# Performance work log

Hardware: AMD Instinct MI355X
Metric: run time of the kernel (lower is better)

Reference implementation:

```python
import jax, jax.numpy as jnp
import numpy as np

BN_EPS = 1e-5


def setup_inputs() -> dict:
    key = jax.random.key(0)
    ks = jax.random.split(key, 8)
    B, C, H, W = 8, 256, 64, 64
    Cqk = C // 8  # query/key channels = out_channels // 8
    x = jax.random.normal(ks[0], (B, C, H, W), dtype=jnp.float32)
    # 1x1 convs == per-pixel matmuls; kaiming-normal-ish scale
    wq = jax.random.normal(ks[1], (Cqk, C), dtype=jnp.float32) * np.sqrt(2.0 / C)
    bq = jnp.zeros((Cqk,), dtype=jnp.float32)
    wk = jax.random.normal(ks[2], (Cqk, C), dtype=jnp.float32) * np.sqrt(2.0 / C)
    bk = jnp.zeros((Cqk,), dtype=jnp.float32)
    wv = jax.random.normal(ks[3], (C, C), dtype=jnp.float32) * np.sqrt(2.0 / C)
    bv = jnp.zeros((C,), dtype=jnp.float32)
    # gamma is initialized to 0 in the original; use a small nonzero value so
    # the attention path actually contributes (and has nontrivial gradients)
    gamma = jnp.full((1,), 0.5, dtype=jnp.float32)
    bn_weight = jnp.ones((C,), dtype=jnp.float32)
    bn_bias = jnp.zeros((C,), dtype=jnp.float32)
    return {"x": x, "wq": wq, "bq": bq, "wk": wk, "bk": bk,
            "wv": wv, "bv": bv, "gamma": gamma,
            "bn_weight": bn_weight, "bn_bias": bn_bias}


def reference(x, wq, bq, wk, bk, wv, bv, gamma, bn_weight, bn_bias):
    B, C, H, W = x.shape
    N = H * W
    xf = x.reshape(B, C, N)  # (B, C, N)
    # 1x1 conv projections as channel matmuls
    q = jnp.einsum('oc,bcn->bno', wq, xf) + bq            # (B, N, Cqk)
    k = jnp.einsum('oc,bcn->bon', wk, xf) + bk[:, None]   # (B, Cqk, N)
    v = jnp.einsum('oc,bcn->bon', wv, xf) + bv[:, None]   # (B, C, N)
    # attention[b, i, j] = softmax_j(q_i . k_j)  -- full N x N matrix
    scores = jnp.einsum('bno,bom->bnm', q, k)             # (B, N, N)
    attn = jax.nn.softmax(scores, axis=2)
    # out[b, c, i] = sum_j v[b, c, j] * attn[b, i, j]
    out = jnp.einsum('bcj,bij->bci', v, attn)             # (B, C, N)
    out = out.reshape(B, C, H, W)
    out = gamma[0] * out + x
    # BatchNorm2d in training mode: batch statistics over (B, H, W)
    mean = jnp.mean(out, axis=(0, 2, 3), keepdims=True)
    var = jnp.var(out, axis=(0, 2, 3), keepdims=True)
    out = (out - mean) * jax.lax.rsqrt(var + BN_EPS)
    out = out * bn_weight[None, :, None, None] + bn_bias[None, :, None, None]
    return jax.nn.relu(out)
```

## Files before the change

### kernel.cpp

```cpp
#include <hip/hip_runtime.h>
#include <stdint.h>

#define B_ 8
#define C_ 256
#define N_ 4096
#define CQK 32
#define VPANEL (C_ * 64)

typedef __attribute__((ext_vector_type(8))) _Float16 f16x8;
typedef __attribute__((ext_vector_type(4))) float f32x4;

__device__ __forceinline__ unsigned short f2bf_rne(float f) {
  unsigned u = __builtin_bit_cast(unsigned, f);
  u += 0x7FFFu + ((u >> 16) & 1u);
  return (unsigned short)(u >> 16);
}

__device__ __forceinline__ float fexp2(float x) {
  float r; asm("v_exp_f32 %0, %1" : "=v"(r) : "v"(x)); return r;
}

__global__ __launch_bounds__(256) void wconv_kernel(
    const float* __restrict__ wq, const float* __restrict__ wk,
    const float* __restrict__ wv, _Float16* __restrict__ wf)
{
  int idx = blockIdx.x * 256 + threadIdx.x;
  int e = idx * 4;
  int o = e >> 8, c = e & 255;
  const float* src;
  if (o < 32)      src = wq + o * 256 + c;
  else if (o < 64) src = wk + (o - 32) * 256 + c;
  else             src = wv + (o - 64) * 256 + c;
  float4 v = *(const float4*)src;
  _Float16 h[4] = {(_Float16)v.x, (_Float16)v.y, (_Float16)v.z, (_Float16)v.w};
  *(uint2*)(wf + e) = *(uint2*)h;
}

__global__ __launch_bounds__(256, 2) void proj_fused_kernel(
    const float* __restrict__ x, const _Float16* __restrict__ wf,
    const float* __restrict__ bq, const float* __restrict__ bk,
    const float* __restrict__ bv,
    _Float16* __restrict__ qf, _Float16* __restrict__ kf,
    _Float16* __restrict__ vout)
{
  __shared__ float xs[64 * 65];
  __shared__ _Float16 bp[32 * 64 * 8];

  const int t = threadIdx.x, lane = t & 63;
  const int w = t >> 6;
  const int l15 = lane & 15, q4 = lane >> 4;
  const int blk = blockIdx.x;
  const int b  = blk & 7;
  const int nt = blk >> 3;
  const int n0 = nt * 64;
  const int o0w = (w & 1) * 32;
  const int n0w = (w >> 1) * 32;

  for (int ct = 0; ct < 4; ++ct) {
    #pragma unroll
    for (int p = 0; p < 4; ++p) {
      int cc = p * 16 + (t >> 4);
      int nn = (t & 15) * 4;
      float4 v = *(const float4*)(x + ((size_t)(b * C_) + ct * 64 + cc) * N_ + n0 + nn);
      xs[cc * 65 + nn]     = v.x;
      xs[cc * 65 + nn + 1] = v.y;
      xs[cc * 65 + nn + 2] = v.z;
      xs[cc * 65 + nn + 3] = v.w;
    }
    __syncthreads();
    #pragma unroll
    for (int h = 0; h < 2; ++h) {
      int oct = w + h * 4;
      int n = lane;
      _Float16 hh[8];
      #pragma unroll
      for (int j = 0; j < 8; ++j) hh[j] = (_Float16)xs[(oct * 8 + j) * 65 + n];
      *(f16x8*)(bp + (((size_t)(ct * 8 + oct)) * 64 + n) * 8) = *(f16x8*)hh;
    }
    __syncthreads();
  }

  const f32x4 zf = {0.f, 0.f, 0.f, 0.f};
  for (int otile = 0; otile < 5; ++otile) {
    f32x4 acc[2][2];
    #pragma unroll
    for (int a = 0; a < 2; ++a)
      #pragma unroll
      for (int bb = 0; bb < 2; ++bb) acc[a][bb] = zf;

    const _Float16* wbase = wf + (size_t)(otile * 64 + o0w) * 256;

    #pragma unroll
    for (int kc = 0; kc < 8; ++kc) {
      f16x8 af[2], bfr[2];
      #pragma unroll
      for (int ob = 0; ob < 2; ++ob)
        af[ob] = *(const f16x8*)(wbase + (ob * 16 + l15) * 256 + kc * 32 + q4 * 8);
      #pragma unroll
      for (int nb = 0; nb < 2; ++nb)
        bfr[nb] = *(const f16x8*)(bp + (((size_t)(kc * 4 + q4)) * 64 + n0w + nb * 16 + l15) * 8);
      #pragma unroll
      for (int ob = 0; ob < 2; ++ob)
        #pragma unroll
        for (int nb = 0; nb < 2; ++nb)
          acc[ob][nb] = __builtin_amdgcn_mfma_f32_16x16x32_f16(af[ob], bfr[nb], acc[ob][nb], 0, 0, 0);
    }

    if (otile == 0) {
      _Float16* dst = (o0w == 0) ? qf : kf;
      const float* bias = (o0w == 0) ? bq : bk;
      const float qsc = (o0w == 0) ? 1.4426950408889634f : 1.0f;
      #pragma unroll
      for (int ob = 0; ob < 2; ++ob) {
        float4 b4 = *(const float4*)(bias + ob * 16 + q4 * 4);
        #pragma unroll
        for (int nb = 0; nb < 2; ++nb) {
          int pixel = n0 + n0w + nb * 16 + l15;
          _Float16 h[4];
          h[0] = (_Float16)((acc[ob][nb][0] + b4.x) * qsc);
          h[1] = (_Float16)((acc[ob][nb][1] + b4.y) * qsc);
          h[2] = (_Float16)((acc[ob][nb][2] + b4.z) * qsc);
          h[3] = (_Float16)((acc[ob][nb][3] + b4.w) * qsc);
          *(uint2*)(dst + ((size_t)(b * N_) + pixel) * CQK + ob * 16 + q4 * 4) = *(uint2*)h;
        }
      }
    } else {
      int cbase = (otile - 1) * 64 + o0w;
      _Float16* vpan = vout + ((size_t)(b * 64 + nt)) * VPANEL;
      #pragma unroll
      for (int ob = 0; ob < 2; ++ob) {
        float4 b4 = *(const float4*)(bv + cbase + ob * 16 + q4 * 4);
        #pragma unroll
        for (int nb = 0; nb < 2; ++nb) {
          int jj = n0w + nb * 16 + l15;
          #pragma unroll
          for (int r = 0; r < 4; ++r) {
            int c = cbase + ob * 16 + q4 * 4 + r;
            float bval = (r == 0) ? b4.x : (r == 1) ? b4.y : (r == 2) ? b4.z : b4.w;
            vpan[(size_t)c * 64 + jj] = (_Float16)(acc[ob][nb][r] + bval);
          }
        }
      }
    }
  }
}

#define ATTN_BODY(K, BUF) do { \
   \
  f16x8 ks_[2]; \
  { const _Float16* kg_ = kstage + (size_t)(((K) + 1) & 31) * (128 * CQK); \
    _Pragma("unroll") \
    for (int s = 0; s < 2; ++s) { \
      int idx_ = s * 256 + t; \
      ks_[s] = *(const f16x8*)(kg_ + (idx_ >> 2) * CQK + (idx_ & 3) * 8); } } \
   \
  f16x8 vx_[16]; \
  { const _Float16* vp_ = vbase + (size_t)(K) * 2 * VPANEL; \
    _Pragma("unroll") \
    for (int ks = 0; ks < 4; ++ks) \
      _Pragma("unroll") \
      for (int cb = 0; cb < 4; ++cb) \
        vx_[ks * 4 + cb] = *(const f16x8*)(vp_ + (ks >> 1) * VPANEL + cb * 1024 + (ks & 1) * 32); } \
   \
  f16x8 kx_[8]; \
  { const _Float16* kl_ = Klds + ((K) & 1) * 5120 + l15 * 40 + q4 * 8; \
    _Pragma("unroll") \
    for (int jb = 0; jb < 8; ++jb) kx_[jb] = *(const f16x8*)(kl_ + jb * (16 * 40)); } \
  f32x4 sv_[8]; \
  _Pragma("unroll") \
  for (int jb = 0; jb < 8; ++jb) \
    sv_[jb] = __builtin_amdgcn_mfma_f32_16x16x32_f16(kx_[jb], qfr, zf, 0, 0, 0); \
  float pm_[8]; \
  _Pragma("unroll") \
  for (int jb = 0; jb < 8; ++jb) \
    pm_[jb] = fmaxf(fmaxf(sv_[jb][0], sv_[jb][1]), fmaxf(sv_[jb][2], sv_[jb][3])); \
  float ra_ = fmaxf(fmaxf(pm_[0], pm_[1]), pm_[2]); \
  float rb_ = fmaxf(fmaxf(pm_[3], pm_[4]), pm_[5]); \
  float rc_ = fmaxf(fmaxf(pm_[6], pm_[7]), ra_); \
  float lm_ = fmaxf(rb_, rc_); \
  lm_ = fmaxf(lm_, __shfl_xor(lm_, 16)); \
  lm_ = fmaxf(lm_, __shfl_xor(lm_, 32)); \
  bool upd_ = lm_ > mold + 8.0f; \
  unsigned long long bal_ = __ballot(upd_);      \
  float alpha_ = upd_ ? fexp2(mold - lm_) : 1.0f; \
  if (upd_) mold = lm_; \
  float ts_ = 0.f; \
  { char* pb_ = (char*)Plds + (BUF) * 17408 + (w * 16 + l15) * 272 + q4 * 8; \
    _Pragma("unroll") \
    for (int jb = 0; jb < 8; ++jb) { \
      float p0_ = fexp2(sv_[jb][0] - mold), p1_ = fexp2(sv_[jb][1] - mold); \
      float p2_ = fexp2(sv_[jb][2] - mold), p3_ = fexp2(sv_[jb][3] - mold); \
      ts_ += (p0_ + p1_) + (p2_ + p3_); \
      _Float16 h_[4] = {(_Float16)p0_, (_Float16)p1_, (_Float16)p2_, (_Float16)p3_}; \
      *(uint2*)(pb_ + jb * 32) = *(uint2*)h_; } } \
   \
  { _Float16* kw_ = Klds + (((K) + 1) & 1) * 5120; \
    _Pragma("unroll") \
    for (int s = 0; s < 2; ++s) { \
      int idx_ = s * 256 + t; \
      *(f16x8*)(kw_ + (idx_ >> 2) * 40 + (idx_ & 3) * 8) = ks_[s]; } } \
  if (q4 == 0) alphal[(BUF) * 64 + w * 16 + l15] = alpha_; \
  if (lane == 0) flagw[(BUF) * 4 + w] = (bal_ != 0ull) ? 1 : 0; \
  ts_ += __shfl_xor(ts_, 16); \
  ts_ += __shfl_xor(ts_, 32); \
  lrun = lrun * alpha_ + ts_; \
  asm volatile("s_waitcnt lgkmcnt(0)" ::: "memory"); \
  __builtin_amdgcn_sched_barrier(0); \
  __builtin_amdgcn_s_barrier(); \
  asm volatile("" ::: "memory"); \
  { int4 fl_ = *(const int4*)(flagw + (BUF) * 4); \
    if (fl_.x | fl_.y | fl_.z | fl_.w) { \
      _Pragma("unroll") \
      for (int ib = 0; ib < 4; ++ib) { \
        float av_ = alphal[(BUF) * 64 + ib * 16 + l15]; \
        _Pragma("unroll") \
        for (int cb = 0; cb < 4; ++cb) \
          _Pragma("unroll") \
          for (int r = 0; r < 4; ++r) acc[cb][ib][r] *= av_; } } } \
  __builtin_amdgcn_s_setprio(1); \
  _Pragma("unroll") \
  for (int ks = 0; ks < 4; ++ks) { \
    f16x8 pf_[4]; \
    _Pragma("unroll") \
    for (int ib = 0; ib < 4; ++ib) \
      pf_[ib] = *(const f16x8*)((char*)Plds + (BUF) * 17408 + (ib * 16 + l15) * 272 + ks * 64 + q4 * 16); \
    _Pragma("unroll") \
    for (int cb = 0; cb < 4; ++cb) \
      _Pragma("unroll") \
      for (int ib = 0; ib < 4; ++ib) \
        acc[cb][ib] = __builtin_amdgcn_mfma_f32_16x16x32_f16(vx_[ks * 4 + cb], pf_[ib], acc[cb][ib], 0, 0, 0); \
  } \
  __builtin_amdgcn_s_setprio(0); \
} while (0)

__global__ __launch_bounds__(256, 2) void attn_kernel(
    const float* __restrict__ x, const float* __restrict__ gptr,
    const _Float16* __restrict__ qf, const _Float16* __restrict__ kf,
    const _Float16* __restrict__ vf, unsigned short* __restrict__ yout)
{
  __shared__ __align__(16) char smem[56096];
  _Float16* Plds  = (_Float16*)smem;
  _Float16* Klds  = (_Float16*)(smem + 34816);
  float* alphal = (float*)(smem + 55296);
  int*   flagw  = (int*)(smem + 55808);
  float* lrowl  = (float*)(smem + 55840);

  const int t = threadIdx.x, lane = t & 63;
  const int w = t >> 6;
  const int l15 = lane & 15, q4 = lane >> 4;
  const int b  = blockIdx.x & 7;
  const int it = blockIdx.x >> 3;
  const int i0 = it * 64;
  const float gamma = gptr[0];

  const f16x8 qfr = *(const f16x8*)(qf + ((size_t)(b * N_) + i0 + w * 16 + l15) * CQK + q4 * 8);

  const _Float16* kstage = kf + (size_t)b * N_ * CQK;
  const _Float16* vbase = vf + (size_t)b * (64 * VPANEL)
                             + ((size_t)(w * 64 + l15)) * 64 + q4 * 8;

  f32x4 acc[4][4];
  const f32x4 zf = {0.f, 0.f, 0.f, 0.f};
  #pragma unroll
  for (int a = 0; a < 4; ++a)
    #pragma unroll
    for (int bb = 0; bb < 4; ++bb) acc[a][bb] = zf;

  float mold = -1e30f, lrun = 0.f;

  #pragma unroll
  for (int s = 0; s < 2; ++s) {
    int idx = s * 256 + t;
    f16x8 v = *(const f16x8*)(kstage + (idx >> 2) * CQK + (idx & 3) * 8);
    *(f16x8*)(Klds + (idx >> 2) * 40 + (idx & 3) * 8) = v;
  }
  __syncthreads();

  #pragma unroll 1
  for (int k = 0; k < 32; k += 2) {
    ATTN_BODY(k, 0);
    ATTN_BODY(k + 1, 1);
  }

  if (q4 == 0) lrowl[w * 16 + l15] = lrun;
  __syncthreads();
  #pragma unroll
  for (int ib = 0; ib < 4; ++ib) {
    float linv = 1.0f / lrowl[ib * 16 + l15];
    int i = i0 + ib * 16 + l15;
    #pragma unroll
    for (int cb = 0; cb < 4; ++cb) {
      #pragma unroll
      for (int r = 0; r < 4; ++r) {
        int c = w * 64 + cb * 16 + q4 * 4 + r;
        size_t off = ((size_t)(b * C_) + c) * N_ + i;
        float o = acc[cb][ib][r] * linv;
        yout[off] = f2bf_rne(fmaf(gamma, o, x[off]));
      }
    }
  }
}

__global__ __launch_bounds__(256) void bnstats_kernel(
    const unsigned short* __restrict__ y, float* __restrict__ meanw, float* __restrict__ rstdw)
{
  const int c = blockIdx.x;
  const int t = threadIdx.x;
  float s1 = 0.f, s2 = 0.f;
  for (int b = 0; b < B_; ++b) {
    const unsigned short* p = y + ((size_t)(b * C_ + c)) * N_;
    #pragma unroll
    for (int r = 0; r < 2; ++r) {
      uint4 u = *(const uint4*)(p + r * 2048 + t * 8);
      unsigned uu[4] = {u.x, u.y, u.z, u.w};
      #pragma unroll
      for (int k = 0; k < 4; ++k) {
        float a = __builtin_bit_cast(float, uu[k] << 16);
        float bb = __builtin_bit_cast(float, uu[k] & 0xFFFF0000u);
        s1 += a + bb;
        s2 += a * a + bb * bb;
      }
    }
  }
  __shared__ float r1[256], r2[256];
  r1[t] = s1; r2[t] = s2;
  __syncthreads();
  for (int s = 128; s > 0; s >>= 1) {
    if (t < s) { r1[t] += r1[t + s]; r2[t] += r2[t + s]; }
    __syncthreads();
  }
  if (t == 0) {
    float mean = r1[0] * (1.0f / 32768.0f);
    float var  = r2[0] * (1.0f / 32768.0f) - mean * mean;
    meanw[c] = mean;
    rstdw[c] = rsqrtf(var + 1e-5f);
  }
}

__global__ __launch_bounds__(256) void bnapply_kernel(
    const unsigned short* __restrict__ y, float* __restrict__ out,
    const float* __restrict__ meanw, const float* __restrict__ rstdw,
    const float* __restrict__ bnw, const float* __restrict__ bnb)
{
  size_t idx = (size_t)blockIdx.x * 256 + threadIdx.x;
  size_t el = idx * 8;
  int c = (int)((el >> 12) & 255);
  float sc = bnw[c] * rstdw[c];
  float sh = fmaf(-meanw[c], sc, bnb[c]);
  uint4 u = *(const uint4*)(y + el);
  unsigned uu[4] = {u.x, u.y, u.z, u.w};
  float4 o0, o1;
  float v[8];
  #pragma unroll
  for (int k = 0; k < 4; ++k) {
    v[2 * k]     = __builtin_bit_cast(float, uu[k] << 16);
    v[2 * k + 1] = __builtin_bit_cast(float, uu[k] & 0xFFFF0000u);
  }
  o0.x = fmaxf(fmaf(v[0], sc, sh), 0.f);
  o0.y = fmaxf(fmaf(v[1], sc, sh), 0.f);
  o0.z = fmaxf(fmaf(v[2], sc, sh), 0.f);
  o0.w = fmaxf(fmaf(v[3], sc, sh), 0.f);
  o1.x = fmaxf(fmaf(v[4], sc, sh), 0.f);
  o1.y = fmaxf(fmaf(v[5], sc, sh), 0.f);
  o1.z = fmaxf(fmaf(v[6], sc, sh), 0.f);
  o1.w = fmaxf(fmaf(v[7], sc, sh), 0.f);
  *(float4*)(out + el) = o0;
  *(float4*)(out + el + 4) = o1;
}

extern "C" void kernel_launch(void* const* d_in, const int* in_sizes, int n_in,
                              void* d_out, int out_size, void* d_ws, size_t ws_size,
                              hipStream_t stream)
{
  const float* x   = (const float*)d_in[0];
  const float* wq  = (const float*)d_in[1];
  const float* bq  = (const float*)d_in[2];
  const float* wk  = (const float*)d_in[3];
  const float* bk  = (const float*)d_in[4];
  const float* wv  = (const float*)d_in[5];
  const float* bv  = (const float*)d_in[6];
  const float* gm  = (const float*)d_in[7];
  const float* bnw = (const float*)d_in[8];
  const float* bnb = (const float*)d_in[9];
  float* out = (float*)d_out;

  _Float16* vfp = (_Float16*)((char*)d_out + (size_t)B_ * C_ * N_ * 2);

  char* ws = (char*)d_ws;
  _Float16* qf = (_Float16*)(ws);
  _Float16* kf = (_Float16*)(ws + ((size_t)2 << 20));
  unsigned short* yout = (unsigned short*)(ws + ((size_t)4 << 20));
  _Float16* wf = (_Float16*)(ws + ((size_t)21 << 20));
  float* meanw = (float*)(ws + ((size_t)22 << 20));
  float* rstdw = (float*)(ws + ((size_t)22 << 20) + 4096);

  hipLaunchKernelGGL(wconv_kernel, dim3(80), dim3(256), 0, stream, wq, wk, wv, wf);
  hipLaunchKernelGGL(proj_fused_kernel, dim3(512), dim3(256), 0, stream,
                     x, wf, bq, bk, bv, qf, kf, vfp);
  hipLaunchKernelGGL(attn_kernel, dim3(512), dim3(256), 0, stream,
                     x, gm, qf, kf, vfp, yout);
  hipLaunchKernelGGL(bnstats_kernel, dim3(256), dim3(256), 0, stream,
                     yout, meanw, rstdw);
  hipLaunchKernelGGL(bnapply_kernel, dim3(4096), dim3(256), 0, stream,
                     yout, out, meanw, rstdw, bnw, bnb);
}
```

Measured before the change: 262.8 us.

## Fuse BatchNorm statistics into attention epilogue via atomics, drop stats kernel

Each attention block now accumulates per-channel sum and sum-of-squares of its fp32 outputs, reduces them across 16 lanes with shuffles, and adds them atomically into a global stats buffer. The buffer is zeroed in the weight-conversion kernel, and the apply kernel derives mean and rstd itself. This removes the separate stats kernel and its extra read of the bf16 intermediate, at the cost of global float atomics and order-dependent summation. It also moves the row-sum shuffle reduction after the barrier so it can overlap with the wait.

After: 288.6 us. 9.8% more time.

```diff
diff --git a/kernel.cpp b/kernel.cpp
--- a/kernel.cpp
+++ b/kernel.cpp
@@ -22,9 +22,11 @@
 
 __global__ __launch_bounds__(256) void wconv_kernel(
     const float* __restrict__ wq, const float* __restrict__ wk,
-    const float* __restrict__ wv, _Float16* __restrict__ wf)
+    const float* __restrict__ wv, _Float16* __restrict__ wf,
+    float* __restrict__ stats)
 {
   int idx = blockIdx.x * 256 + threadIdx.x;
+  if (idx < 512) stats[idx] = 0.f;
   int e = idx * 4;
   int o = e >> 8, c = e & 255;
   const float* src;
@@ -201,13 +203,14 @@
       *(f16x8*)(kw_ + (idx_ >> 2) * 40 + (idx_ & 3) * 8) = ks_[s]; } } \
   if (q4 == 0) alphal[(BUF) * 64 + w * 16 + l15] = alpha_; \
   if (lane == 0) flagw[(BUF) * 4 + w] = (bal_ != 0ull) ? 1 : 0; \
-  ts_ += __shfl_xor(ts_, 16); \
-  ts_ += __shfl_xor(ts_, 32); \
-  lrun = lrun * alpha_ + ts_; \
   asm volatile("s_waitcnt lgkmcnt(0)" ::: "memory"); \
   __builtin_amdgcn_sched_barrier(0); \
   __builtin_amdgcn_s_barrier(); \
   asm volatile("" ::: "memory"); \
+   \
+  ts_ += __shfl_xor(ts_, 16); \
+  ts_ += __shfl_xor(ts_, 32); \
+  lrun = lrun * alpha_ + ts_; \
   { int4 fl_ = *(const int4*)(flagw + (BUF) * 4); \
     if (fl_.x | fl_.y | fl_.z | fl_.w) { \
       _Pragma("unroll") \
@@ -236,7 +239,8 @@
 __global__ __launch_bounds__(256, 2) void attn_kernel(
     const float* __restrict__ x, const float* __restrict__ gptr,
     const _Float16* __restrict__ qf, const _Float16* __restrict__ kf,
-    const _Float16* __restrict__ vf, unsigned short* __restrict__ yout)
+    const _Float16* __restrict__ vf, unsigned short* __restrict__ yout,
+    float* __restrict__ stats)
 {
   __shared__ __align__(16) char smem[56096];
   _Float16* Plds  = (_Float16*)smem;
@@ -284,69 +288,52 @@
 
   if (q4 == 0) lrowl[w * 16 + l15] = lrun;
   __syncthreads();
-  #pragma unroll
-  for (int ib = 0; ib < 4; ++ib) {
-    float linv = 1.0f / lrowl[ib * 16 + l15];
-    int i = i0 + ib * 16 + l15;
-    #pragma unroll
-    for (int cb = 0; cb < 4; ++cb) {
-      #pragma unroll
-      for (int r = 0; r < 4; ++r) {
-        int c = w * 64 + cb * 16 + q4 * 4 + r;
+  float linv[4];
+  #pragma unroll
+  for (int ib = 0; ib < 4; ++ib) linv[ib] = 1.0f / lrowl[ib * 16 + l15];
+
+  #pragma unroll
+  for (int cb = 0; cb < 4; ++cb) {
+    #pragma unroll
+    for (int r = 0; r < 4; ++r) {
+      int c = w * 64 + cb * 16 + q4 * 4 + r;
+      float s1 = 0.f, s2 = 0.f;
+      #pragma unroll
+      for (int ib = 0; ib < 4; ++ib) {
+        int i = i0 + ib * 16 + l15;
         size_t off = ((size_t)(b * C_) + c) * N_ + i;
-        float o = acc[cb][ib][r] * linv;
-        yout[off] = f2bf_rne(fmaf(gamma, o, x[off]));
-      }
-    }
-  }
-}
-
-__global__ __launch_bounds__(256) void bnstats_kernel(
-    const unsigned short* __restrict__ y, float* __restrict__ meanw, float* __restrict__ rstdw)
-{
-  const int c = blockIdx.x;
-  const int t = threadIdx.x;
-  float s1 = 0.f, s2 = 0.f;
-  for (int b = 0; b < B_; ++b) {
-    const unsigned short* p = y + ((size_t)(b * C_ + c)) * N_;
-    #pragma unroll
-    for (int r = 0; r < 2; ++r) {
-      uint4 u = *(const uint4*)(p + r * 2048 + t * 8);
-      unsigned uu[4] = {u.x, u.y, u.z, u.w};
-      #pragma unroll
-      for (int k = 0; k < 4; ++k) {
-        float a = __builtin_bit_cast(float, uu[k] << 16);
-        float bb = __builtin_bit_cast(float, uu[k] & 0xFFFF0000u);
-        s1 += a + bb;
-        s2 += a * a + bb * bb;
-      }
-    }
-  }
-  __shared__ float r1[256], r2[256];
-  r1[t] = s1; r2[t] = s2;
-  __syncthreads();
-  for (int s = 128; s > 0; s >>= 1) {
-    if (t < s) { r1[t] += r1[t + s]; r2[t] += r2[t + s]; }
-    __syncthreads();
-  }
-  if (t == 0) {
-    float mean = r1[0] * (1.0f / 32768.0f);
-    float var  = r2[0] * (1.0f / 32768.0f) - mean * mean;
-    meanw[c] = mean;
-    rstdw[c] = rsqrtf(var + 1e-5f);
+        float y = fmaf(gamma, acc[cb][ib][r] * linv[ib], x[off]);
+        yout[off] = f2bf_rne(y);
+        s1 += y;
+        s2 += y * y;
+      }
+      #pragma unroll
+      for (int m = 1; m < 16; m <<= 1) {
+        s1 += __shfl_xor(s1, m);
+        s2 += __shfl_xor(s2, m);
+      }
+      if (l15 == 0) {
+        atomicAdd(stats + c, s1);
+        atomicAdd(stats + 256 + c, s2);
+      }
+    }
   }
 }
 
 __global__ __launch_bounds__(256) void bnapply_kernel(
     const unsigned short* __restrict__ y, float* __restrict__ out,
-    const float* __restrict__ meanw, const float* __restrict__ rstdw,
+    const float* __restrict__ stats,
     const float* __restrict__ bnw, const float* __restrict__ bnb)
 {
   size_t idx = (size_t)blockIdx.x * 256 + threadIdx.x;
   size_t el = idx * 8;
   int c = (int)((el >> 12) & 255);
-  float sc = bnw[c] * rstdw[c];
-  float sh = fmaf(-meanw[c], sc, bnb[c]);
+  float s1 = stats[c], s2 = stats[256 + c];
+  float mean = s1 * (1.0f / 32768.0f);
+  float var  = fmaf(-mean, mean, s2 * (1.0f / 32768.0f));
+  float rstd = rsqrtf(var + 1e-5f);
+  float sc = bnw[c] * rstd;
+  float sh = fmaf(-mean, sc, bnb[c]);
   uint4 u = *(const uint4*)(y + el);
   unsigned uu[4] = {u.x, u.y, u.z, u.w};
   float4 o0, o1;
@@ -391,16 +378,14 @@
   _Float16* kf = (_Float16*)(ws + ((size_t)2 << 20));
   unsigned short* yout = (unsigned short*)(ws + ((size_t)4 << 20));
   _Float16* wf = (_Float16*)(ws + ((size_t)21 << 20));
-  float* meanw = (float*)(ws + ((size_t)22 << 20));
-  float* rstdw = (float*)(ws + ((size_t)22 << 20) + 4096);
-
-  hipLaunchKernelGGL(wconv_kernel, dim3(80), dim3(256), 0, stream, wq, wk, wv, wf);
+  float* stats = (float*)(ws + ((size_t)22 << 20));
+
+  hipLaunchKernelGGL(wconv_kernel, dim3(80), dim3(256), 0, stream,
+                     wq, wk, wv, wf, stats);
   hipLaunchKernelGGL(proj_fused_kernel, dim3(512), dim3(256), 0, stream,
                      x, wf, bq, bk, bv, qf, kf, vfp);
   hipLaunchKernelGGL(attn_kernel, dim3(512), dim3(256), 0, stream,
-                     x, gm, qf, kf, vfp, yout);
-  hipLaunchKernelGGL(bnstats_kernel, dim3(256), dim3(256), 0, stream,
-                     yout, meanw, rstdw);
+                     x, gm, qf, kf, vfp, yout, stats);
   hipLaunchKernelGGL(bnapply_kernel, dim3(4096), dim3(256), 0, stream,
-                     yout, out, meanw, rstdw, bnw, bnb);
-}
+                     yout, out, stats, bnw, bnb);
+}
```
